# Kernel tuning notes

Measured on AMD Instinct MI355X. Metric: run time of the kernel, lower is better.

## Reference

```python
import jax, jax.numpy as jnp
import numpy as np

S, B, H = 1024, 4, 1024
NH, NC = 16, 4            # num_attention_heads, num_combined_heads
HPH = H // NH             # 64
NF = NH // NC             # num_FFN = 4
FFM = 8                   # combined_FFN_multiple
DIN = NC * HPH            # 256, grouped FFN input dim
DHID = FFM * DIN          # 2048, dense_in output dim
DH2 = DHID // 2           # 1024, GLU half / dense_out input dim
EPS = 1e-6
NORM_FACTOR = 1.0 / float(np.sqrt(HPH))


def _ln(x, g, b):
    m = x.mean(-1, keepdims=True)
    v = ((x - m) ** 2).mean(-1, keepdims=True)
    return (x - m) * jax.lax.rsqrt(v + EPS) * g + b


def setup_inputs() -> dict:
    key = jax.random.key(0)
    ks = jax.random.split(key, 10)
    p = lambda k, shape: jax.random.normal(k, shape, jnp.float32) * 0.02
    return {
        "hidden_states": jax.random.normal(ks[0], (S, B, H), jnp.float32),
        "g1": jnp.ones((H,), jnp.float32), "b1": jnp.zeros((H,), jnp.float32),
        "g2": jnp.ones((HPH,), jnp.float32), "b2": jnp.zeros((HPH,), jnp.float32),
        "Wq": p(ks[1], (H, H)), "bq": jnp.zeros((H,), jnp.float32),
        "Wk": p(ks[2], (H, H)), "bk": jnp.zeros((H,), jnp.float32),
        "Wv": p(ks[3], (H, H)), "bv": jnp.zeros((H,), jnp.float32),
        "W_in": p(ks[4], (NF, DIN, DHID)), "b_in": jnp.zeros((NF, DHID), jnp.float32),
        "W_out": p(ks[5], (NF, DH2, DIN)), "b_out": jnp.zeros((NF, DIN), jnp.float32),
        "Wd": p(ks[6], (H, H)), "bd": jnp.zeros((H,), jnp.float32),
    }


def reference(hidden_states, g1, b1, g2, b2, Wq, bq, Wk, bk, Wv, bv,
              W_in, b_in, W_out, b_out, Wd, bd):
    # hidden_states: [S, B, H]
    x = _ln(hidden_states, g1, b1)                       # norm1

    def heads(t):  # [S,B,H] -> [B*NH, S, HPH] (matches view + transpose in torch)
        return jnp.transpose(t.reshape(S, B * NH, HPH), (1, 0, 2))

    q = heads(x @ Wq + bq)
    k = heads(x @ Wk + bk)
    v = heads(x @ Wv + bv)

    # subtraction_gaussian_kernel: pairwise squared euclidean distance
    qk = jnp.einsum('nsd,ntd->nst', q, k)                # [B*NH, S, S]
    q2 = jnp.sum(q * q, axis=-1)
    k2 = jnp.sum(k * k, axis=-1)
    dist = q2[:, :, None] + k2[None if False else slice(None), None, :][0] if False else q2[:, :, None] + k2[:, None, :] - 2.0 * qk
    matmul_result = dist * (-0.5 * NORM_FACTOR)          # scores <= 0

    # Exp sequence op: elementwise exp (softmax replacement, no normalization)
    probs = jnp.exp(matmul_result)

    ctx = jnp.einsum('nst,ntd->nsd', probs, v)           # [B*NH, S, HPH]
    ctx = jnp.transpose(ctx, (1, 0, 2)).reshape(S, B, H)
    ctx = x + ctx                                        # residual with norm1 output (as in source)

    ctx = _ln(ctx.reshape(S, B, NH, HPH), g2, b2)        # per-head norm2

    # grouped FFN over contiguous head subsets (vectorized over the NF groups)
    cg = ctx.reshape(S, B, NF, DIN)
    h = jnp.einsum('sbgi,gio->sbgo', cg, W_in) + b_in    # [S,B,NF,DHID]
    xh, yh = jnp.split(h, 2, axis=-1)
    h = xh * jax.nn.relu(yh)                             # GLU-style x * relu(y)
    og = jnp.einsum('sbgi,gio->sbgo', h, W_out) + b_out  # [S,B,NF,DIN]

    out = og.reshape(S, B, H) @ Wd + bd                  # attention_dense
    return out, matmul_result
```

## Files before the change

### kernel.cpp

```cpp
#include <hip/hip_runtime.h>


typedef __attribute__((ext_vector_type(8))) short short8;
typedef __attribute__((ext_vector_type(4))) float f32x4;

__device__ __forceinline__ unsigned short f2bf(float f) {
  union { float f; unsigned u; } x; x.f = f;
  unsigned r = x.u + 0x7FFFu + ((x.u >> 16) & 1u);
  return (unsigned short)(r >> 16);
}
__device__ __forceinline__ float bf2f(unsigned short u) {
  union { float f; unsigned u; } x; x.u = ((unsigned)u) << 16;
  return x.f;
}
__device__ __forceinline__ unsigned cvtpk(float a, float b) {
  unsigned r;
  asm("v_cvt_pk_bf16_f32 %0, %1, %2" : "=v"(r) : "v"(a), "v"(b));
  return r;
}
__device__ __forceinline__ void gload16(const unsigned short* g, unsigned short* l) {
  __builtin_amdgcn_global_load_lds(
      (const __attribute__((address_space(1))) unsigned int*)g,
      (__attribute__((address_space(3))) unsigned int*)l, 16, 0, 0);
}

__global__ __launch_bounds__(256) void ln1_kernel(
    const float* __restrict__ x, const float* __restrict__ g,
    const float* __restrict__ b, float* __restrict__ y,
    unsigned short* __restrict__ ybf)
{
  const long base = (long)blockIdx.x * 1024;
  const int c = threadIdx.x * 4;
  float4 v = *(const float4*)(x + base + c);
  float s = v.x + v.y + v.z + v.w;
  float ss = v.x*v.x + v.y*v.y + v.z*v.z + v.w*v.w;
  #pragma unroll
  for (int off = 32; off > 0; off >>= 1) {
    s  += __shfl_xor(s, off);
    ss += __shfl_xor(ss, off);
  }
  __shared__ float sw[4], ssw[4];
  const int wave = threadIdx.x >> 6;
  if ((threadIdx.x & 63) == 0) { sw[wave] = s; ssw[wave] = ss; }
  __syncthreads();
  s  = sw[0] + sw[1] + sw[2] + sw[3];
  ss = ssw[0] + ssw[1] + ssw[2] + ssw[3];
  const float mean = s * (1.0f/1024.0f);
  const float var  = ss * (1.0f/1024.0f) - mean*mean;
  const float rs   = rsqrtf(var + 1e-6f);
  const float4 gv = *(const float4*)(g + c);
  const float4 bv = *(const float4*)(b + c);
  float4 o;
  o.x = (v.x - mean) * rs * gv.x + bv.x;
  o.y = (v.y - mean) * rs * gv.y + bv.y;
  o.z = (v.z - mean) * rs * gv.z + bv.z;
  o.w = (v.w - mean) * rs * gv.w + bv.w;
  *(float4*)(y + base + c) = o;
  ushort4 ob;
  ob.x = f2bf(o.x); ob.y = f2bf(o.y); ob.z = f2bf(o.z); ob.w = f2bf(o.w);
  *(ushort4*)(ybf + base + c) = ob;
}

__device__ __forceinline__ void transpose_body(
    const float* __restrict__ Wg, unsigned short* __restrict__ WTg,
    int K, int N, int bx, int by, int tid)
{
  __shared__ float T[32][33];
  const int n0 = bx * 32, k0 = by * 32;
  const int r = tid >> 3, c4 = (tid & 7) * 4;
  float4 v = *(const float4*)(Wg + (long)(k0 + r) * N + n0 + c4);
  T[r][c4+0] = v.x; T[r][c4+1] = v.y; T[r][c4+2] = v.z; T[r][c4+3] = v.w;
  __syncthreads();
  ushort4 o;
  o.x = f2bf(T[c4+0][r]); o.y = f2bf(T[c4+1][r]);
  o.z = f2bf(T[c4+2][r]); o.w = f2bf(T[c4+3][r]);
  *(ushort4*)(WTg + (long)(n0 + r) * K + k0 + c4) = o;
}

__global__ __launch_bounds__(256) void prep_weights_kernel(
    const float* __restrict__ Wq, const float* __restrict__ Wk,
    const float* __restrict__ Wv, const float* __restrict__ Wd,
    const float* __restrict__ Win, const float* __restrict__ Wout,
    const float* __restrict__ bq, const float* __restrict__ bk,
    const float* __restrict__ bv,
    unsigned short* __restrict__ wqkvT, unsigned short* __restrict__ wdT,
    unsigned short* __restrict__ winT, unsigned short* __restrict__ woutT,
    float* __restrict__ qkvb)
{
  const int idx = blockIdx.x;
  const int tid = threadIdx.x;
  if (idx < 4096) {
    const int z = idx >> 10, rem = idx & 1023;
    const float* W = (z == 0) ? Wq : (z == 1) ? Wk : (z == 2) ? Wv : Wd;
    unsigned short* WT = (z == 3) ? wdT : wqkvT + (long)z * 1048576;
    transpose_body(W, WT, 1024, 1024, rem & 31, rem >> 5, tid);
  } else if (idx < 6144) {
    const int rem = idx - 4096;
    const int z = rem >> 9, r2 = rem & 511;
    transpose_body(Win + (long)z * 524288, winT + (long)z * 524288,
                   256, 2048, r2 & 63, r2 >> 6, tid);
  } else if (idx < 7168) {
    const int rem = idx - 6144;
    const int z = rem >> 8, r2 = rem & 255;
    transpose_body(Wout + (long)z * 262144, woutT + (long)z * 262144,
                   1024, 256, r2 & 7, r2 >> 3, tid);
  } else {
    const int i = (idx - 7168) * 256 + tid;
    qkvb[i] = (i < 1024) ? bq[i] : ((i < 2048) ? bk[i - 1024] : bv[i - 2048]);
  }
}

__global__ __launch_bounds__(256) void mfma_gemm_kernel(
    const unsigned short* __restrict__ A, int lda, long agoff,
    const unsigned short* __restrict__ BT, long bgoff, int K,
    const float* __restrict__ bias, int biasoff,
    unsigned short* __restrict__ Cbf, float* __restrict__ Cf,
    int ldc, int cgoff)
{
  const int g = blockIdx.z;
  const unsigned short* Ag = A + (long)g * agoff;
  const unsigned short* Bg = BT + (long)g * bgoff;
  const float* biasg = bias + (long)g * biasoff;
  const int row0 = blockIdx.y * 128, col0 = blockIdx.x * 128;
  __shared__ __align__(16) unsigned short As[2][128 * 64];
  __shared__ __align__(16) unsigned short Bs[2][128 * 64];
  const int tid = threadIdx.x;
  const int w = tid >> 6, l = tid & 63;
  const int ms = (w & 1) << 6, ns = (w >> 1) << 6;
  const int fr = l & 15, fg = l >> 4;
  const int lr8 = l >> 3, ls8 = l & 7;
  const int scol = (ls8 ^ lr8) << 3;
  const int rsw = fr & 7;
  f32x4 acc[4][4];
  #pragma unroll
  for (int i = 0; i < 4; ++i)
    #pragma unroll
    for (int j = 0; j < 4; ++j) acc[i][j] = (f32x4)0.0f;

  const int nt = K >> 6;
  #pragma unroll
  for (int sidx = 0; sidx < 2; ++sidx) {
    const int k0 = sidx << 6;
    #pragma unroll
    for (int g8 = 0; g8 < 4; ++g8) {
      const int r = (w << 5) + (g8 << 3);
      gload16(Ag + (long)(row0 + r + lr8) * lda + k0 + scol, &As[sidx][r * 64]);
      gload16(Bg + (long)(col0 + r + lr8) * K  + k0 + scol, &Bs[sidx][r * 64]);
    }
  }
  int cur = 0;
  for (int t = 0; t < nt; ++t) {
    if (t + 1 < nt) asm volatile("s_waitcnt vmcnt(8)" ::: "memory");
    else            asm volatile("s_waitcnt vmcnt(0)" ::: "memory");
    __builtin_amdgcn_s_barrier();
    __builtin_amdgcn_sched_barrier(0);
    short8 af[2][4], bfr[2][4];
    #pragma unroll
    for (int ks = 0; ks < 2; ++ks) {
      const int rslot = (((ks << 2) + fg) ^ rsw) << 3;
      #pragma unroll
      for (int i = 0; i < 4; ++i) {
        af[ks][i]  = *(const short8*)&As[cur][(ms + i*16 + fr) * 64 + rslot];
        bfr[ks][i] = *(const short8*)&Bs[cur][(ns + i*16 + fr) * 64 + rslot];
      }
    }
    asm volatile("s_waitcnt lgkmcnt(0)" ::: "memory");
    __builtin_amdgcn_sched_barrier(0);
    __builtin_amdgcn_s_barrier();
    if (t + 2 < nt) {
      const int k0 = (t + 2) << 6;
      #pragma unroll
      for (int g8 = 0; g8 < 4; ++g8) {
        const int r = (w << 5) + (g8 << 3);
        gload16(Ag + (long)(row0 + r + lr8) * lda + k0 + scol, &As[cur][r * 64]);
        gload16(Bg + (long)(col0 + r + lr8) * K  + k0 + scol, &Bs[cur][r * 64]);
      }
    }
    __builtin_amdgcn_s_setprio(1);
    #pragma unroll
    for (int ks = 0; ks < 2; ++ks)
      #pragma unroll
      for (int i = 0; i < 4; ++i)
        #pragma unroll
        for (int j = 0; j < 4; ++j)
          acc[i][j] = __builtin_amdgcn_mfma_f32_16x16x32_bf16(bfr[ks][j], af[ks][i], acc[i][j], 0, 0, 0);
    __builtin_amdgcn_s_setprio(0);
    cur ^= 1;
  }

  #pragma unroll
  for (int j = 0; j < 4; ++j) {
    const float4 bj4 = *(const float4*)(biasg + col0 + ns + j*16 + (fg << 2));
    #pragma unroll
    for (int i = 0; i < 4; ++i) {
      const long row = row0 + ms + i*16 + fr;
      const long cb = row * ldc + (long)g * cgoff + col0 + ns + j*16 + (fg << 2);
      const float v0 = acc[i][j][0] + bj4.x, v1 = acc[i][j][1] + bj4.y;
      const float v2 = acc[i][j][2] + bj4.z, v3 = acc[i][j][3] + bj4.w;
      if (Cbf) {
        uint2 pk; pk.x = cvtpk(v0, v1); pk.y = cvtpk(v2, v3);
        *(uint2*)(Cbf + cb) = pk;
      } else {
        f32x4 o = {v0, v1, v2, v3};
        __builtin_nontemporal_store(o, (f32x4*)(Cf + cb));
      }
    }
  }
}

__global__ __launch_bounds__(256) void mfma_gemm64_kernel(
    const unsigned short* __restrict__ A, int lda, long agoff,
    const unsigned short* __restrict__ BT, long bgoff, int K,
    const float* __restrict__ bias, int biasoff,
    unsigned short* __restrict__ Cbf, float* __restrict__ Cf,
    int ldc, int cgoff)
{
  const int g = blockIdx.z;
  const unsigned short* Ag = A + (long)g * agoff;
  const unsigned short* Bg = BT + (long)g * bgoff;
  const float* biasg = bias + (long)g * biasoff;
  const int row0 = blockIdx.y * 128, col0 = blockIdx.x * 64;
  __shared__ __align__(16) unsigned short As[2][128 * 64];
  __shared__ __align__(16) unsigned short Bs[2][64 * 64];
  const int tid = threadIdx.x;
  const int w = tid >> 6, l = tid & 63;
  const int ms = (w & 1) << 6, ns = (w >> 1) << 5;
  const int fr = l & 15, fg = l >> 4;
  const int lr8 = l >> 3, ls8 = l & 7;
  const int scol = (ls8 ^ lr8) << 3;
  const int rsw = fr & 7;
  f32x4 acc[4][2];
  #pragma unroll
  for (int i = 0; i < 4; ++i)
    #pragma unroll
    for (int j = 0; j < 2; ++j) acc[i][j] = (f32x4)0.0f;

  const int nt = K >> 6;
  #pragma unroll
  for (int sidx = 0; sidx < 2; ++sidx) {
    const int k0 = sidx << 6;
    #pragma unroll
    for (int g8 = 0; g8 < 4; ++g8) {
      const int r = (w << 5) + (g8 << 3);
      gload16(Ag + (long)(row0 + r + lr8) * lda + k0 + scol, &As[sidx][r * 64]);
    }
    #pragma unroll
    for (int g8 = 0; g8 < 2; ++g8) {
      const int r = (w << 4) + (g8 << 3);
      gload16(Bg + (long)(col0 + r + lr8) * K + k0 + scol, &Bs[sidx][r * 64]);
    }
  }
  int cur = 0;
  for (int t = 0; t < nt; ++t) {
    if (t + 1 < nt) asm volatile("s_waitcnt vmcnt(6)" ::: "memory");
    else            asm volatile("s_waitcnt vmcnt(0)" ::: "memory");
    __builtin_amdgcn_s_barrier();
    __builtin_amdgcn_sched_barrier(0);
    short8 af[2][4], bfr[2][2];
    #pragma unroll
    for (int ks = 0; ks < 2; ++ks) {
      const int rslot = (((ks << 2) + fg) ^ rsw) << 3;
      #pragma unroll
      for (int i = 0; i < 4; ++i)
        af[ks][i] = *(const short8*)&As[cur][(ms + i*16 + fr) * 64 + rslot];
      #pragma unroll
      for (int j = 0; j < 2; ++j)
        bfr[ks][j] = *(const short8*)&Bs[cur][(ns + j*16 + fr) * 64 + rslot];
    }
    asm volatile("s_waitcnt lgkmcnt(0)" ::: "memory");
    __builtin_amdgcn_sched_barrier(0);
    __builtin_amdgcn_s_barrier();
    if (t + 2 < nt) {
      const int k0 = (t + 2) << 6;
      #pragma unroll
      for (int g8 = 0; g8 < 4; ++g8) {
        const int r = (w << 5) + (g8 << 3);
        gload16(Ag + (long)(row0 + r + lr8) * lda + k0 + scol, &As[cur][r * 64]);
      }
      #pragma unroll
      for (int g8 = 0; g8 < 2; ++g8) {
        const int r = (w << 4) + (g8 << 3);
        gload16(Bg + (long)(col0 + r + lr8) * K + k0 + scol, &Bs[cur][r * 64]);
      }
    }
    __builtin_amdgcn_s_setprio(1);
    #pragma unroll
    for (int ks = 0; ks < 2; ++ks)
      #pragma unroll
      for (int i = 0; i < 4; ++i)
        #pragma unroll
        for (int j = 0; j < 2; ++j)
          acc[i][j] = __builtin_amdgcn_mfma_f32_16x16x32_bf16(bfr[ks][j], af[ks][i], acc[i][j], 0, 0, 0);
    __builtin_amdgcn_s_setprio(0);
    cur ^= 1;
  }

  #pragma unroll
  for (int j = 0; j < 2; ++j) {
    const float4 bj4 = *(const float4*)(biasg + col0 + ns + j*16 + (fg << 2));
    #pragma unroll
    for (int i = 0; i < 4; ++i) {
      const long row = row0 + ms + i*16 + fr;
      const long cb = row * ldc + (long)g * cgoff + col0 + ns + j*16 + (fg << 2);
      const float v0 = acc[i][j][0] + bj4.x, v1 = acc[i][j][1] + bj4.y;
      const float v2 = acc[i][j][2] + bj4.z, v3 = acc[i][j][3] + bj4.w;
      if (Cbf) {
        uint2 pk; pk.x = cvtpk(v0, v1); pk.y = cvtpk(v2, v3);
        *(uint2*)(Cbf + cb) = pk;
      } else {
        f32x4 o = {v0, v1, v2, v3};
        __builtin_nontemporal_store(o, (f32x4*)(Cf + cb));
      }
    }
  }
}

__global__ __launch_bounds__(256) void mfma_glu_kernel(
    const unsigned short* __restrict__ A,
    const unsigned short* __restrict__ WT,
    const float* __restrict__ bin,
    unsigned short* __restrict__ H2)
{
  const int g = blockIdx.z;
  const unsigned short* Ag = A + g * 256;
  const unsigned short* Wg = WT + (long)g * 2048 * 256;
  const float* bg = bin + g * 2048;
  const int row0 = blockIdx.y * 128, col0 = blockIdx.x * 64;
  __shared__ __align__(16) unsigned short As[2][128 * 64];
  __shared__ __align__(16) unsigned short Bxs[2][64 * 64];
  __shared__ __align__(16) unsigned short Bys[2][64 * 64];
  const int tid = threadIdx.x;
  const int w = tid >> 6, l = tid & 63;
  const int ms = (w & 1) << 6, ns = (w >> 1) << 5;
  const int fr = l & 15, fg = l >> 4;
  const int lr8 = l >> 3, ls8 = l & 7;
  const int scol = (ls8 ^ lr8) << 3;
  const int rsw = fr & 7;
  f32x4 ax[4][2], ay[4][2];
  #pragma unroll
  for (int i = 0; i < 4; ++i)
    #pragma unroll
    for (int j = 0; j < 2; ++j) { ax[i][j] = (f32x4)0.0f; ay[i][j] = (f32x4)0.0f; }

  #pragma unroll
  for (int sidx = 0; sidx < 2; ++sidx) {
    const int k0 = sidx << 6;
    #pragma unroll
    for (int g8 = 0; g8 < 4; ++g8) {
      const int r = (w << 5) + (g8 << 3);
      gload16(Ag + (long)(row0 + r + lr8) * 1024 + k0 + scol, &As[sidx][r * 64]);
    }
    #pragma unroll
    for (int g8 = 0; g8 < 2; ++g8) {
      const int r = (w << 4) + (g8 << 3);
      gload16(Wg + (long)(col0 + r + lr8) * 256 + k0 + scol,        &Bxs[sidx][r * 64]);
      gload16(Wg + (long)(1024 + col0 + r + lr8) * 256 + k0 + scol, &Bys[sidx][r * 64]);
    }
  }
  int cur = 0;
  for (int t = 0; t < 4; ++t) {
    if (t + 1 < 4) asm volatile("s_waitcnt vmcnt(8)" ::: "memory");
    else           asm volatile("s_waitcnt vmcnt(0)" ::: "memory");
    __builtin_amdgcn_s_barrier();
    __builtin_amdgcn_sched_barrier(0);
    short8 af[2][4], bx[2][2], by[2][2];
    #pragma unroll
    for (int ks = 0; ks < 2; ++ks) {
      const int rslot = (((ks << 2) + fg) ^ rsw) << 3;
      #pragma unroll
      for (int i = 0; i < 4; ++i)
        af[ks][i] = *(const short8*)&As[cur][(ms + i*16 + fr) * 64 + rslot];
      #pragma unroll
      for (int j = 0; j < 2; ++j) {
        bx[ks][j] = *(const short8*)&Bxs[cur][(ns + j*16 + fr) * 64 + rslot];
        by[ks][j] = *(const short8*)&Bys[cur][(ns + j*16 + fr) * 64 + rslot];
      }
    }
    asm volatile("s_waitcnt lgkmcnt(0)" ::: "memory");
    __builtin_amdgcn_sched_barrier(0);
    __builtin_amdgcn_s_barrier();
    if (t + 2 < 4) {
      const int k0 = (t + 2) << 6;
      #pragma unroll
      for (int g8 = 0; g8 < 4; ++g8) {
        const int r = (w << 5) + (g8 << 3);
        gload16(Ag + (long)(row0 + r + lr8) * 1024 + k0 + scol, &As[cur][r * 64]);
      }
      #pragma unroll
      for (int g8 = 0; g8 < 2; ++g8) {
        const int r = (w << 4) + (g8 << 3);
        gload16(Wg + (long)(col0 + r + lr8) * 256 + k0 + scol,        &Bxs[cur][r * 64]);
        gload16(Wg + (long)(1024 + col0 + r + lr8) * 256 + k0 + scol, &Bys[cur][r * 64]);
      }
    }
    __builtin_amdgcn_s_setprio(1);
    #pragma unroll
    for (int ks = 0; ks < 2; ++ks)
      #pragma unroll
      for (int i = 0; i < 4; ++i)
        #pragma unroll
        for (int j = 0; j < 2; ++j) {
          ax[i][j] = __builtin_amdgcn_mfma_f32_16x16x32_bf16(bx[ks][j], af[ks][i], ax[i][j], 0, 0, 0);
          ay[i][j] = __builtin_amdgcn_mfma_f32_16x16x32_bf16(by[ks][j], af[ks][i], ay[i][j], 0, 0, 0);
        }
    __builtin_amdgcn_s_setprio(0);
    cur ^= 1;
  }

  #pragma unroll
  for (int j = 0; j < 2; ++j) {
    const float4 bx4 = *(const float4*)(bg + col0 + ns + j*16 + (fg << 2));
    const float4 by4 = *(const float4*)(bg + 1024 + col0 + ns + j*16 + (fg << 2));
    #pragma unroll
    for (int i = 0; i < 4; ++i) {
      const long row = row0 + ms + i*16 + fr;
      const long cb = row * 4096 + g * 1024 + col0 + ns + j*16 + (fg << 2);
      float o4[4];
      const float* bxp = &bx4.x; const float* byp = &by4.x;
      #pragma unroll
      for (int r4 = 0; r4 < 4; ++r4) {
        const float xh = ax[i][j][r4] + bxp[r4];
        const float yh = ay[i][j][r4] + byp[r4];
        o4[r4] = xh * fmaxf(yh, 0.0f);
      }
      uint2 pk; pk.x = cvtpk(o4[0], o4[1]); pk.y = cvtpk(o4[2], o4[3]);
      *(uint2*)(H2 + cb) = pk;
    }
  }
}

__global__ __launch_bounds__(256) void prep_attn_kernel(
    const unsigned short* __restrict__ qkv,
    float* __restrict__ q2g, float* __restrict__ k2g,
    unsigned short* __restrict__ vt)
{
  const int n = blockIdx.y, s0 = blockIdx.x * 64;
  const int b = n >> 4, hoff = (n & 15) * 64;
  const int tid = threadIdx.x;
  __shared__ unsigned short T[64][72];
  #pragma unroll
  for (int p = 0; p < 2; ++p) {
    const int r = (tid >> 3) + p * 32, c = (tid & 7) << 3;
    *(short8*)&T[r][c] = *(const short8*)(qkv + ((long)((s0 + r) * 4 + b)) * 3072 + 2048 + hoff + c);
  }
  {
    const int r = tid >> 2, e = tid & 3;
    const long base = ((long)((s0 + r) * 4 + b)) * 3072 + hoff + (e << 4);
    float sq = 0.f, sk = 0.f;
    #pragma unroll
    for (int ch = 0; ch < 2; ++ch) {
      short8 q8 = *(const short8*)(qkv + base + (ch << 3));
      short8 k8 = *(const short8*)(qkv + base + 1024 + (ch << 3));
      #pragma unroll
      for (int ee = 0; ee < 8; ++ee) {
        float f = bf2f((unsigned short)q8[ee]); sq = fmaf(f, f, sq);
        f = bf2f((unsigned short)k8[ee]); sk = fmaf(f, f, sk);
      }
    }
    sq += __shfl_xor(sq, 1); sq += __shfl_xor(sq, 2);
    sk += __shfl_xor(sk, 1); sk += __shfl_xor(sk, 2);
    if (e == 0) {
      q2g[n * 1024 + s0 + r] = sq;
      k2g[n * 1024 + s0 + r] = sk;
    }
  }
  __syncthreads();
  #pragma unroll
  for (int p = 0; p < 2; ++p) {
    const int d = (tid >> 3) + p * 32, sc = (tid & 7) << 3;
    short8 o;
    #pragma unroll
    for (int j = 0; j < 8; ++j) o[j] = (short)T[sc + j][d];
    *(short8*)(vt + ((long)n * 64 + d) * 1024 + s0 + sc) = o;
  }
}

__global__ __launch_bounds__(256) void attn_kernel(
    const unsigned short* __restrict__ qkv, const unsigned short* __restrict__ vt,
    const float* __restrict__ q2g, const float* __restrict__ k2g,
    const float* __restrict__ xln, const float* __restrict__ g2,
    const float* __restrict__ b2,
    unsigned short* __restrict__ ctx2, float* __restrict__ scores)
{
  const int n = blockIdx.y;
  const int s0 = blockIdx.x * 64;
  const int b = n >> 4, hoff = (n & 15) * 64;
  __shared__ __align__(16) unsigned short Qs[64][72];
  __shared__ __align__(16) unsigned short Ks[2][64 * 64];
  __shared__ __align__(16) unsigned short VTl[2][64 * 64];
  __shared__ __align__(16) unsigned short Ps[64][72];
  const int tid = threadIdx.x, w = tid >> 6, l = tid & 63;
  const int fr = l & 15, fg = l >> 4;
  const int lr8 = l >> 3, ls8 = l & 7;
  const int sslot = ((ls8 ^ lr8) << 3);
  const int rsw = fr & 7;

  #pragma unroll
  for (int p = 0; p < 2; ++p) {
    const int r = (tid >> 3) + p * 32, c = (tid & 7) << 3;
    *(short8*)&Qs[r][c] = *(const short8*)(qkv + ((long)((s0 + r) * 4 + b)) * 3072 + hoff + c);
  }
  float q2m[4];
  #pragma unroll
  for (int i = 0; i < 4; ++i) q2m[i] = -0.0625f * q2g[n * 1024 + s0 + i*16 + fr];

  #pragma unroll
  for (int p = 0; p < 2; ++p) {
    const int rowb = p * 32 + w * 8;
    gload16(qkv + ((long)((rowb + lr8) * 4 + b)) * 3072 + 1024 + hoff + sslot, &Ks[0][rowb * 64]);
    gload16(vt + ((long)n * 64 + rowb + lr8) * 1024 + sslot,                   &VTl[0][rowb * 64]);
  }
  __syncthreads();

  f32x4 o[4];
  #pragma unroll
  for (int i = 0; i < 4; ++i) o[i] = (f32x4)0.0f;

  int cur = 0;
  for (int t0 = 0; t0 < 1024; t0 += 64) {
    if (t0 + 64 < 1024) {
      #pragma unroll
      for (int p = 0; p < 2; ++p) {
        const int rowb = p * 32 + w * 8;
        gload16(qkv + ((long)((t0 + 64 + rowb + lr8) * 4 + b)) * 3072 + 1024 + hoff + sslot,
                &Ks[cur ^ 1][rowb * 64]);
        gload16(vt + ((long)n * 64 + rowb + lr8) * 1024 + t0 + 64 + sslot,
                &VTl[cur ^ 1][rowb * 64]);
      }
    }
    const float4 k2v4 = *(const float4*)(k2g + n * 1024 + t0 + (w << 4) + (fg << 2));
    const float k2m[4] = {-0.0625f*k2v4.x, -0.0625f*k2v4.y, -0.0625f*k2v4.z, -0.0625f*k2v4.w};

    f32x4 c4[4];
    #pragma unroll
    for (int i = 0; i < 4; ++i) c4[i] = (f32x4)0.0f;
    #pragma unroll
    for (int ks = 0; ks < 2; ++ks) {
      const short8 kf = *(const short8*)&Ks[cur][((w << 4) + fr) * 64 + ((((ks << 2) + fg) ^ rsw) << 3)];
      #pragma unroll
      for (int i = 0; i < 4; ++i) {
        const short8 qf = *(const short8*)&Qs[i*16 + fr][(ks << 5) + (fg << 3)];
        c4[i] = __builtin_amdgcn_mfma_f32_16x16x32_bf16(kf, qf, c4[i], 0, 0, 0);
      }
    }
    #pragma unroll
    for (int i = 0; i < 4; ++i) {
      f32x4 sc;
      float pe[4];
      #pragma unroll
      for (int r4 = 0; r4 < 4; ++r4) {
        const float m = fmaf(c4[i][r4], 0.125f, q2m[i] + k2m[r4]);
        sc[r4] = m;
        pe[r4] = __expf(m);
      }
      __builtin_nontemporal_store(sc,
          (f32x4*)(scores + (long)n * 1048576 + (long)(s0 + i*16 + fr) * 1024 + t0 + (w << 4) + (fg << 2)));
      uint2 pk; pk.x = cvtpk(pe[0], pe[1]); pk.y = cvtpk(pe[2], pe[3]);
      *(uint2*)&Ps[i*16 + fr][(w << 4) + (fg << 2)] = pk;
    }
    __syncthreads();

    #pragma unroll
    for (int ks = 0; ks < 2; ++ks) {
      const short8 vb = *(const short8*)&VTl[cur][((w << 4) + fr) * 64 + ((((ks << 2) + fg) ^ rsw) << 3)];
      #pragma unroll
      for (int i = 0; i < 4; ++i) {
        const short8 pf = *(const short8*)&Ps[i*16 + fr][(ks << 5) + (fg << 3)];
        o[i] = __builtin_amdgcn_mfma_f32_16x16x32_bf16(vb, pf, o[i], 0, 0, 0);
      }
    }
    __syncthreads();
    cur ^= 1;
  }

  const int dbase = (w << 4) + (fg << 2);
  float4 xl4[4];
  #pragma unroll
  for (int i = 0; i < 4; ++i)
    xl4[i] = *(const float4*)(xln + ((long)((s0 + i*16 + fr) * 4 + b)) * 1024 + hoff + dbase);

  float* redbuf = (float*)&Ps[0][0];
  const int slot = (w << 2) + fg;
  #pragma unroll
  for (int i = 0; i < 4; ++i) {
    float s = 0.f, ss = 0.f;
    const float* xp = &xl4[i].x;
    #pragma unroll
    for (int r4 = 0; r4 < 4; ++r4) {
      const float v = o[i][r4] + xp[r4];
      s += v; ss = fmaf(v, v, ss);
    }
    redbuf[(i*16 + fr) * 16 + slot] = s;
    redbuf[1024 + (i*16 + fr) * 16 + slot] = ss;
  }
  __syncthreads();
  float* statbuf = (float*)&Qs[0][0];
  {
    const int row = tid >> 2, q4 = tid & 3;
    float s = 0.f, ss = 0.f;
    #pragma unroll
    for (int k = 0; k < 4; ++k) {
      s  += redbuf[row * 16 + q4 * 4 + k];
      ss += redbuf[1024 + row * 16 + q4 * 4 + k];
    }
    s  += __shfl_xor(s, 1);  s  += __shfl_xor(s, 2);
    ss += __shfl_xor(ss, 1); ss += __shfl_xor(ss, 2);
    if (q4 == 0) {
      const float mean = s * (1.0f/64.0f);
      const float var  = ss * (1.0f/64.0f) - mean * mean;
      statbuf[row] = mean;
      statbuf[64 + row] = rsqrtf(var + 1e-6f);
    }
  }
  __syncthreads();
  const float4 g2v = *(const float4*)(g2 + dbase);
  const float4 b2v = *(const float4*)(b2 + dbase);
  const float* gp = &g2v.x; const float* bp = &b2v.x;
  #pragma unroll
  for (int i = 0; i < 4; ++i) {
    const float mean = statbuf[i*16 + fr];
    const float rs   = statbuf[64 + i*16 + fr];
    const float* xp = &xl4[i].x;
    float vo[4];
    #pragma unroll
    for (int r4 = 0; r4 < 4; ++r4)
      vo[r4] = (o[i][r4] + xp[r4] - mean) * rs * gp[r4] + bp[r4];
    uint2 pk; pk.x = cvtpk(vo[0], vo[1]); pk.y = cvtpk(vo[2], vo[3]);
    *(uint2*)(ctx2 + ((long)((s0 + i*16 + fr) * 4 + b)) * 1024 + hoff + dbase) = pk;
  }
}

extern "C" void kernel_launch(void* const* d_in, const int* in_sizes, int n_in,
                              void* d_out, int out_size, void* d_ws, size_t ws_size,
                              hipStream_t stream) {
  const float* hs   = (const float*)d_in[0];
  const float* g1   = (const float*)d_in[1];
  const float* b1   = (const float*)d_in[2];
  const float* g2   = (const float*)d_in[3];
  const float* b2   = (const float*)d_in[4];
  const float* Wq   = (const float*)d_in[5];
  const float* bq   = (const float*)d_in[6];
  const float* Wk   = (const float*)d_in[7];
  const float* bk   = (const float*)d_in[8];
  const float* Wv   = (const float*)d_in[9];
  const float* bv   = (const float*)d_in[10];
  const float* Win  = (const float*)d_in[11];
  const float* bin  = (const float*)d_in[12];
  const float* Wout = (const float*)d_in[13];
  const float* bout = (const float*)d_in[14];
  const float* Wd   = (const float*)d_in[15];
  const float* bd   = (const float*)d_in[16];

  char* ws = (char*)d_ws;
  float*          xln   = (float*)(ws + 0);
  unsigned short* xbf   = (unsigned short*)(ws + 16777216);
  unsigned short* qkv   = (unsigned short*)(ws + 25165824);
  unsigned short* ctx2  = (unsigned short*)(ws + 67108864);
  unsigned short* wqkvT = (unsigned short*)(ws + 75497472);
  unsigned short* winT  = (unsigned short*)(ws + 81788928);
  unsigned short* woutT = (unsigned short*)(ws + 85983232);
  unsigned short* wdT   = (unsigned short*)(ws + 88080384);
  float*          qkvb  = (float*)(ws + 90177536);
  unsigned short* vt    = (unsigned short*)(ws + 90189824);
  float*          q2g   = (float*)(ws + 98578432);
  float*          k2g   = (float*)(ws + 98840576);
  unsigned short* h2    = (unsigned short*)(ws + 16777216);
  unsigned short* og    = (unsigned short*)(ws + 0);

  float* out0 = (float*)d_out;
  float* out1 = out0 + 4194304;

  ln1_kernel<<<4096, 256, 0, stream>>>(hs, g1, b1, xln, xbf);

  prep_weights_kernel<<<7180, 256, 0, stream>>>(
      Wq, Wk, Wv, Wd, Win, Wout, bq, bk, bv, wqkvT, wdT, winT, woutT, qkvb);

  mfma_gemm_kernel<<<dim3(24,32,1), 256, 0, stream>>>(
      xbf, 1024, 0, wqkvT, 0, 1024, qkvb, 0, qkv, nullptr, 3072, 0);

  prep_attn_kernel<<<dim3(16,64), 256, 0, stream>>>(qkv, q2g, k2g, vt);

  attn_kernel<<<dim3(16,64), 256, 0, stream>>>(qkv, vt, q2g, k2g, xln, g2, b2, ctx2, out1);

  mfma_glu_kernel<<<dim3(16,32,4), 256, 0, stream>>>(ctx2, winT, bin, h2);

  mfma_gemm64_kernel<<<dim3(4,32,4), 256, 0, stream>>>(
      h2, 4096, 1024, woutT, 262144, 1024, bout, 256, og, nullptr, 1024, 256);

  mfma_gemm64_kernel<<<dim3(16,32,1), 256, 0, stream>>>(
      og, 1024, 0, wdT, 0, 1024, bd, 0, nullptr, out0, 1024, 0);
}
```

Baseline: 243.8 us.

## Fuse LN1 into weight prep, compute q/k norms in QKV GEMM, retune attention loop

Merges the LayerNorm kernel into the weight-prep launch, and moves the q²/k² row-norm computation into the QKV GEMM epilogue so that the separate prep kernel only transposes V. In the attention kernel, k² is staged in LDS, Q and P tiles use XOR-swizzled unpadded layouts, and the QK MFMA is issued before the next-tile prefetch. Full syncthreads are replaced with explicit waitcnt plus s_barrier. The norms are now computed from fp32 values rather than bf16-rounded ones, which slightly changes numerics relative to the bf16 q/k used in the dot product. The hand-written vmcnt(4) wait assumes a particular count of outstanding loads.

```diff
diff --git a/kernel.cpp b/kernel.cpp
--- a/kernel.cpp
+++ b/kernel.cpp
@@ -24,13 +24,13 @@
       (__attribute__((address_space(3))) unsigned int*)l, 16, 0, 0);
 }
 
-__global__ __launch_bounds__(256) void ln1_kernel(
+__device__ __forceinline__ void ln1_body(
     const float* __restrict__ x, const float* __restrict__ g,
     const float* __restrict__ b, float* __restrict__ y,
-    unsigned short* __restrict__ ybf)
+    unsigned short* __restrict__ ybf, int row, int tid)
 {
-  const long base = (long)blockIdx.x * 1024;
-  const int c = threadIdx.x * 4;
+  const long base = (long)row * 1024;
+  const int c = tid * 4;
   float4 v = *(const float4*)(x + base + c);
   float s = v.x + v.y + v.z + v.w;
   float ss = v.x*v.x + v.y*v.y + v.z*v.z + v.w*v.w;
@@ -40,8 +40,8 @@
     ss += __shfl_xor(ss, off);
   }
   __shared__ float sw[4], ssw[4];
-  const int wave = threadIdx.x >> 6;
-  if ((threadIdx.x & 63) == 0) { sw[wave] = s; ssw[wave] = ss; }
+  const int wave = tid >> 6;
+  if ((tid & 63) == 0) { sw[wave] = s; ssw[wave] = ss; }
   __syncthreads();
   s  = sw[0] + sw[1] + sw[2] + sw[3];
   ss = ssw[0] + ssw[1] + ssw[2] + ssw[3];
@@ -77,7 +77,10 @@
   *(ushort4*)(WTg + (long)(n0 + r) * K + k0 + c4) = o;
 }
 
-__global__ __launch_bounds__(256) void prep_weights_kernel(
+__global__ __launch_bounds__(256) void prep_all_kernel(
+    const float* __restrict__ hs, const float* __restrict__ g1,
+    const float* __restrict__ b1, float* __restrict__ xln,
+    unsigned short* __restrict__ xbf,
     const float* __restrict__ Wq, const float* __restrict__ Wk,
     const float* __restrict__ Wv, const float* __restrict__ Wd,
     const float* __restrict__ Win, const float* __restrict__ Wout,
@@ -87,25 +90,28 @@
     unsigned short* __restrict__ winT, unsigned short* __restrict__ woutT,
     float* __restrict__ qkvb)
 {
-  const int idx = blockIdx.x;
+  const int bid = blockIdx.x;
   const int tid = threadIdx.x;
-  if (idx < 4096) {
+  if (bid < 4096) {
+    ln1_body(hs, g1, b1, xln, xbf, bid, tid);
+  } else if (bid < 8192) {
+    const int idx = bid - 4096;
     const int z = idx >> 10, rem = idx & 1023;
     const float* W = (z == 0) ? Wq : (z == 1) ? Wk : (z == 2) ? Wv : Wd;
     unsigned short* WT = (z == 3) ? wdT : wqkvT + (long)z * 1048576;
     transpose_body(W, WT, 1024, 1024, rem & 31, rem >> 5, tid);
-  } else if (idx < 6144) {
-    const int rem = idx - 4096;
+  } else if (bid < 10240) {
+    const int rem = bid - 8192;
     const int z = rem >> 9, r2 = rem & 511;
     transpose_body(Win + (long)z * 524288, winT + (long)z * 524288,
                    256, 2048, r2 & 63, r2 >> 6, tid);
-  } else if (idx < 7168) {
-    const int rem = idx - 6144;
+  } else if (bid < 11264) {
+    const int rem = bid - 10240;
     const int z = rem >> 8, r2 = rem & 255;
     transpose_body(Wout + (long)z * 262144, woutT + (long)z * 262144,
                    1024, 256, r2 & 7, r2 >> 3, tid);
   } else {
-    const int i = (idx - 7168) * 256 + tid;
+    const int i = (bid - 11264) * 256 + tid;
     qkvb[i] = (i < 1024) ? bq[i] : ((i < 2048) ? bk[i - 1024] : bv[i - 2048]);
   }
 }
@@ -115,7 +121,8 @@
     const unsigned short* __restrict__ BT, long bgoff, int K,
     const float* __restrict__ bias, int biasoff,
     unsigned short* __restrict__ Cbf, float* __restrict__ Cf,
-    int ldc, int cgoff)
+    int ldc, int cgoff,
+    float* __restrict__ q2g, float* __restrict__ k2g)
 {
   const int g = blockIdx.z;
   const unsigned short* Ag = A + (long)g * agoff;
@@ -188,6 +195,7 @@
     cur ^= 1;
   }
 
+  float s2[4] = {0.f, 0.f, 0.f, 0.f};
   #pragma unroll
   for (int j = 0; j < 4; ++j) {
     const float4 bj4 = *(const float4*)(biasg + col0 + ns + j*16 + (fg << 2));
@@ -197,12 +205,29 @@
       const long cb = row * ldc + (long)g * cgoff + col0 + ns + j*16 + (fg << 2);
       const float v0 = acc[i][j][0] + bj4.x, v1 = acc[i][j][1] + bj4.y;
       const float v2 = acc[i][j][2] + bj4.z, v3 = acc[i][j][3] + bj4.w;
+      s2[i] += v0*v0 + v1*v1 + v2*v2 + v3*v3;
       if (Cbf) {
         uint2 pk; pk.x = cvtpk(v0, v1); pk.y = cvtpk(v2, v3);
         *(uint2*)(Cbf + cb) = pk;
       } else {
         f32x4 o = {v0, v1, v2, v3};
         __builtin_nontemporal_store(o, (f32x4*)(Cf + cb));
+      }
+    }
+  }
+  if (q2g && col0 < 2048) {
+    const int nsAbs = col0 + ns;
+    const bool isQ = nsAbs < 1024;
+    float* outp = isQ ? q2g : k2g;
+    const int head = (isQ ? nsAbs : nsAbs - 1024) >> 6;
+    #pragma unroll
+    for (int i = 0; i < 4; ++i) {
+      float s = s2[i];
+      s += __shfl_xor(s, 16);
+      s += __shfl_xor(s, 32);
+      if (fg == 0) {
+        const int gr = row0 + ms + i*16 + fr;
+        outp[((gr & 3) * 16 + head) * 1024 + (gr >> 2)] = s;
       }
     }
   }
@@ -429,40 +454,17 @@
   }
 }
 
-__global__ __launch_bounds__(256) void prep_attn_kernel(
-    const unsigned short* __restrict__ qkv,
-    float* __restrict__ q2g, float* __restrict__ k2g,
-    unsigned short* __restrict__ vt)
+__global__ __launch_bounds__(256) void vtrans_kernel(
+    const unsigned short* __restrict__ qkv, unsigned short* __restrict__ vt)
 {
+  __shared__ unsigned short T[64][72];
   const int n = blockIdx.y, s0 = blockIdx.x * 64;
   const int b = n >> 4, hoff = (n & 15) * 64;
   const int tid = threadIdx.x;
-  __shared__ unsigned short T[64][72];
   #pragma unroll
   for (int p = 0; p < 2; ++p) {
     const int r = (tid >> 3) + p * 32, c = (tid & 7) << 3;
     *(short8*)&T[r][c] = *(const short8*)(qkv + ((long)((s0 + r) * 4 + b)) * 3072 + 2048 + hoff + c);
-  }
-  {
-    const int r = tid >> 2, e = tid & 3;
-    const long base = ((long)((s0 + r) * 4 + b)) * 3072 + hoff + (e << 4);
-    float sq = 0.f, sk = 0.f;
-    #pragma unroll
-    for (int ch = 0; ch < 2; ++ch) {
-      short8 q8 = *(const short8*)(qkv + base + (ch << 3));
-      short8 k8 = *(const short8*)(qkv + base + 1024 + (ch << 3));
-      #pragma unroll
-      for (int ee = 0; ee < 8; ++ee) {
-        float f = bf2f((unsigned short)q8[ee]); sq = fmaf(f, f, sq);
-        f = bf2f((unsigned short)k8[ee]); sk = fmaf(f, f, sk);
-      }
-    }
-    sq += __shfl_xor(sq, 1); sq += __shfl_xor(sq, 2);
-    sk += __shfl_xor(sk, 1); sk += __shfl_xor(sk, 2);
-    if (e == 0) {
-      q2g[n * 1024 + s0 + r] = sq;
-      k2g[n * 1024 + s0 + r] = sk;
-    }
   }
   __syncthreads();
   #pragma unroll
@@ -485,10 +487,11 @@
   const int n = blockIdx.y;
   const int s0 = blockIdx.x * 64;
   const int b = n >> 4, hoff = (n & 15) * 64;
-  __shared__ __align__(16) unsigned short Qs[64][72];
+  __shared__ __align__(16) unsigned short Qs[64 * 64];
   __shared__ __align__(16) unsigned short Ks[2][64 * 64];
   __shared__ __align__(16) unsigned short VTl[2][64 * 64];
-  __shared__ __align__(16) unsigned short Ps[64][72];
+  __shared__ __align__(16) unsigned short Ps[64 * 64];
+  __shared__ float k2s[1024];
   const int tid = threadIdx.x, w = tid >> 6, l = tid & 63;
   const int fr = l & 15, fg = l >> 4;
   const int lr8 = l >> 3, ls8 = l & 7;
@@ -497,13 +500,14 @@
 
   #pragma unroll
   for (int p = 0; p < 2; ++p) {
-    const int r = (tid >> 3) + p * 32, c = (tid & 7) << 3;
-    *(short8*)&Qs[r][c] = *(const short8*)(qkv + ((long)((s0 + r) * 4 + b)) * 3072 + hoff + c);
-  }
+    const int r = (tid >> 3) + p * 32, cs = tid & 7;
+    *(short8*)&Qs[r * 64 + ((cs ^ (r & 7)) << 3)] =
+        *(const short8*)(qkv + ((long)((s0 + r) * 4 + b)) * 3072 + hoff + (cs << 3));
+  }
+  *(float4*)&k2s[tid << 2] = *(const float4*)(k2g + n * 1024 + (tid << 2));
   float q2m[4];
   #pragma unroll
   for (int i = 0; i < 4; ++i) q2m[i] = -0.0625f * q2g[n * 1024 + s0 + i*16 + fr];
-
   #pragma unroll
   for (int p = 0; p < 2; ++p) {
     const int rowb = p * 32 + w * 8;
@@ -518,6 +522,23 @@
 
   int cur = 0;
   for (int t0 = 0; t0 < 1024; t0 += 64) {
+    if (t0 > 0) {
+      asm volatile("s_waitcnt vmcnt(4)" ::: "memory");
+      __builtin_amdgcn_sched_barrier(0);
+      __builtin_amdgcn_s_barrier();
+    }
+    f32x4 c4[4];
+    #pragma unroll
+    for (int i = 0; i < 4; ++i) c4[i] = (f32x4)0.0f;
+    #pragma unroll
+    for (int ks = 0; ks < 2; ++ks) {
+      const short8 kf = *(const short8*)&Ks[cur][((w << 4) + fr) * 64 + ((((ks << 2) + fg) ^ rsw) << 3)];
+      #pragma unroll
+      for (int i = 0; i < 4; ++i) {
+        const short8 qf = *(const short8*)&Qs[(i*16 + fr) * 64 + ((((ks << 2) + fg) ^ rsw) << 3)];
+        c4[i] = __builtin_amdgcn_mfma_f32_16x16x32_bf16(kf, qf, c4[i], 0, 0, 0);
+      }
+    }
     if (t0 + 64 < 1024) {
       #pragma unroll
       for (int p = 0; p < 2; ++p) {
@@ -528,21 +549,8 @@
                 &VTl[cur ^ 1][rowb * 64]);
       }
     }
-    const float4 k2v4 = *(const float4*)(k2g + n * 1024 + t0 + (w << 4) + (fg << 2));
+    const float4 k2v4 = *(const float4*)&k2s[t0 + (w << 4) + (fg << 2)];
     const float k2m[4] = {-0.0625f*k2v4.x, -0.0625f*k2v4.y, -0.0625f*k2v4.z, -0.0625f*k2v4.w};
-
-    f32x4 c4[4];
-    #pragma unroll
-    for (int i = 0; i < 4; ++i) c4[i] = (f32x4)0.0f;
-    #pragma unroll
-    for (int ks = 0; ks < 2; ++ks) {
-      const short8 kf = *(const short8*)&Ks[cur][((w << 4) + fr) * 64 + ((((ks << 2) + fg) ^ rsw) << 3)];
-      #pragma unroll
-      for (int i = 0; i < 4; ++i) {
-        const short8 qf = *(const short8*)&Qs[i*16 + fr][(ks << 5) + (fg << 3)];
-        c4[i] = __builtin_amdgcn_mfma_f32_16x16x32_bf16(kf, qf, c4[i], 0, 0, 0);
-      }
-    }
     #pragma unroll
     for (int i = 0; i < 4; ++i) {
       f32x4 sc;
@@ -555,21 +563,26 @@
       }
       __builtin_nontemporal_store(sc,
           (f32x4*)(scores + (long)n * 1048576 + (long)(s0 + i*16 + fr) * 1024 + t0 + (w << 4) + (fg << 2)));
+      const int slot = (w << 1) + (fg >> 1);
+      const int pc = ((slot ^ (fr & 7)) << 3) + ((fg & 1) << 2);
       uint2 pk; pk.x = cvtpk(pe[0], pe[1]); pk.y = cvtpk(pe[2], pe[3]);
-      *(uint2*)&Ps[i*16 + fr][(w << 4) + (fg << 2)] = pk;
-    }
-    __syncthreads();
-
+      *(uint2*)&Ps[(i*16 + fr) * 64 + pc] = pk;
+    }
+    asm volatile("s_waitcnt lgkmcnt(0)" ::: "memory");
+    __builtin_amdgcn_sched_barrier(0);
+    __builtin_amdgcn_s_barrier();
     #pragma unroll
     for (int ks = 0; ks < 2; ++ks) {
       const short8 vb = *(const short8*)&VTl[cur][((w << 4) + fr) * 64 + ((((ks << 2) + fg) ^ rsw) << 3)];
       #pragma unroll
       for (int i = 0; i < 4; ++i) {
-        const short8 pf = *(const short8*)&Ps[i*16 + fr][(ks << 5) + (fg << 3)];
+        const short8 pf = *(const short8*)&Ps[(i*16 + fr) * 64 + ((((ks << 2) + fg) ^ rsw) << 3)];
         o[i] = __builtin_amdgcn_mfma_f32_16x16x32_bf16(vb, pf, o[i], 0, 0, 0);
       }
     }
-    __syncthreads();
+    asm volatile("s_waitcnt lgkmcnt(0)" ::: "memory");
+    __builtin_amdgcn_sched_barrier(0);
+    __builtin_amdgcn_s_barrier();
     cur ^= 1;
   }
 
@@ -579,7 +592,7 @@
   for (int i = 0; i < 4; ++i)
     xl4[i] = *(const float4*)(xln + ((long)((s0 + i*16 + fr) * 4 + b)) * 1024 + hoff + dbase);
 
-  float* redbuf = (float*)&Ps[0][0];
+  float* redbuf = (float*)&Ps[0];
   const int slot = (w << 2) + fg;
   #pragma unroll
   for (int i = 0; i < 4; ++i) {
@@ -594,7 +607,7 @@
     redbuf[1024 + (i*16 + fr) * 16 + slot] = ss;
   }
   __syncthreads();
-  float* statbuf = (float*)&Qs[0][0];
+  float* statbuf = (float*)&Qs[0];
   {
     const int row = tid >> 2, q4 = tid & 3;
     float s = 0.f, ss = 0.f;
@@ -670,15 +683,15 @@
   float* out0 = (float*)d_out;
   float* out1 = out0 + 4194304;
 
-  ln1_kernel<<<4096, 256, 0, stream>>>(hs, g1, b1, xln, xbf);
-
-  prep_weights_kernel<<<7180, 256, 0, stream>>>(
-      Wq, Wk, Wv, Wd, Win, Wout, bq, bk, bv, wqkvT, wdT, winT, woutT, qkvb);
+  prep_all_kernel<<<11276, 256, 0, stream>>>(
+      hs, g1, b1, xln, xbf,
+      Wq, Wk, Wv, Wd, Win, Wout, bq, bk, bv,
+      wqkvT, wdT, winT, woutT, qkvb);
 
   mfma_gemm_kernel<<<dim3(24,32,1), 256, 0, stream>>>(
-      xbf, 1024, 0, wqkvT, 0, 1024, qkvb, 0, qkv, nullptr, 3072, 0);
-
-  prep_attn_kernel<<<dim3(16,64), 256, 0, stream>>>(qkv, q2g, k2g, vt);
+      xbf, 1024, 0, wqkvT, 0, 1024, qkvb, 0, qkv, nullptr, 3072, 0, q2g, k2g);
+
+  vtrans_kernel<<<dim3(16,64), 256, 0, stream>>>(qkv, vt);
 
   attn_kernel<<<dim3(16,64), 256, 0, stream>>>(qkv, vt, q2g, k2g, xln, g2, b2, ctx2, out1);
 
```

New measurement: 233.5 us. 1.04x faster.
